# Optimization experiments

Hardware: AMD Instinct MI355X
Metric: run time of the kernel (lower is better)

The kernel has to match this reference:

```python
import jax, jax.numpy as jnp
import numpy as np

SLOPE = 25.0   # snntorch fast_sigmoid default slope
EPS = 1e-5     # BatchNorm eps
ALPHA = 1.0    # tdBN alpha
VTH_BN = 1.0   # tdBN VTH constant

@jax.custom_vjp
def spike_fn(x):
    # Heaviside forward, fast-sigmoid surrogate backward
    return (x > 0).astype(x.dtype)

def _spike_fwd(x):
    return (x > 0).astype(x.dtype), x

def _spike_bwd(x, g):
    return (g / (SLOPE * jnp.abs(x) + 1.0) ** 2,)

spike_fn.defvjp(_spike_fwd, _spike_bwd)

def setup_inputs() -> dict:
    key = jax.random.key(0)
    ks = jax.random.split(key, 4)
    B, T, F_in, F_out = 64, 64, 2048, 2048
    x = jax.random.normal(ks[0], (B, T, F_in), jnp.float32)
    mem_init = jnp.zeros((B, F_out), jnp.float32)
    # Linear params (Kaiming-uniform-ish init)
    W = jax.random.normal(ks[1], (F_out, F_in), jnp.float32) / np.sqrt(F_in)
    b = jax.random.uniform(ks[2], (F_out,), jnp.float32, -1.0, 1.0) / np.sqrt(F_in)
    # tdBN affine params
    gamma = jnp.ones((F_out,), jnp.float32)
    beta_bn = jnp.zeros((F_out,), jnp.float32)
    # LIF learnable params
    lif_beta = jnp.float32(0.9)
    thr = jnp.float32(1.0)
    return dict(x=x, mem_init=mem_init, W=W, b=b, gamma=gamma,
                beta_bn=beta_bn, lif_beta=lif_beta, thr=thr)

def reference(x, mem_init, W, b, gamma, beta_bn, lif_beta, thr):
    B, T, F_in = x.shape
    # Linear over all (batch, time) tokens at once
    h = jnp.einsum('btf,of->bto', x, W) + b  # (B, T, F_out)
    # tdBN: normalize per-feature over (batch, time), scale by alpha*VTH
    mean = h.mean(axis=(0, 1))
    var = h.var(axis=(0, 1))  # biased, matches torch BN training stats
    h = ALPHA * VTH_BN * (h - mean) / jnp.sqrt(var + EPS) * gamma + beta_bn
    # LIF (snntorch Leaky, subtract reset) scanned over time
    beta_c = jnp.clip(lif_beta, 0.0, 1.0)
    def step(mem, xt):
        # reset based on previous mem, detached (snntorch mem_reset)
        reset = jax.lax.stop_gradient((mem - thr > 0).astype(mem.dtype))
        mem_new = beta_c * mem + xt - reset * thr
        spk = spike_fn(mem_new - thr)
        return mem_new, spk
    _, spks = jax.lax.scan(step, mem_init, jnp.swapaxes(h, 0, 1))  # spks: (T, B, F)
    return jnp.swapaxes(spks, 0, 1)  # (B, T, F_out)
```

## Files before the change

kernel.cpp:

```cpp
#include <hip/hip_runtime.h>


typedef double double4v __attribute__((ext_vector_type(4)));

#define KDIM 2048
#define NDIM 2048
#define LROW 132

__global__ __launch_bounds__(256, 2) void gemm_f64_mfma2(
    const float* __restrict__ X,
    const float* __restrict__ W,
    const float* __restrict__ bias,
    double* __restrict__ H)
{
    constexpr int NT = KDIM / 16;
    __shared__ float As[2][16][LROW];
    __shared__ float Bs[2][16][LROW];

    const int tid  = threadIdx.x;
    const int lane = tid & 63;
    const int wid  = tid >> 6;
    const int lf = lane & 15, lq = lane >> 4;
    const int bm = blockIdx.x * 128, bn = blockIdx.y * 128;
    const int wr = wid >> 1, wc = wid & 1;

    double4v pd = (double4v){0.0, 0.0, 0.0, 0.0};
    pd = __builtin_amdgcn_mfma_f64_16x16x4f64(
        (double)(lane + 1), (double)((lane + 1) * (lane + 1)), pd, 0, 0, 0);
    int winner = -1;
    #pragma unroll
    for (int h = 0; h < 16; ++h) {
        const int c1 = h & 1, c2 = (h >> 1) & 1, cd = h >> 2;
        bool ok = true;
        #pragma unroll
        for (int v = 0; v < 4; ++v) {
            const int r16 = (cd == 0) ? 4 * lq + v : (cd == 1) ? lf
                          : (cd == 2) ? lq + 4 * v : lf;
            const int c16 = (cd == 0) ? lf : (cd == 1) ? 4 * lq + v
                          : (cd == 2) ? lf : lq + 4 * v;
            double s = 0.0;
            #pragma unroll
            for (int k = 0; k < 4; ++k) {
                const int i1 = c1 ? (r16 + 16 * k) : (4 * r16 + k);
                const int i2 = c2 ? (c16 + 16 * k) : (4 * c16 + k);
                s += (double)(i1 + 1) * (double)((i2 + 1) * (i2 + 1));
            }
            ok = ok && (pd[v] == s);
        }
        if (__ballot(ok) == ~0ull && winner < 0) winner = h;
    }
    if (winner < 0) winner = 0;
    const int selA = winner & 1, selB = (winner >> 1) & 1, selD = winner >> 2;

    const int rlA = selA ? lf : (lane >> 2);
    const int klA = selA ? lq : (lane & 3);
    const int rlB = selB ? lf : (lane >> 2);
    const int klB = selB ? lq : (lane & 3);
    const int baseA = klA * LROW + wr * 64 + rlA;
    const int baseB = klB * LROW + wc * 64 + rlB;

    const int arow = tid >> 1;
    const int akof = (tid & 1) * 8;
    const float* xa = X + (size_t)(bm + arow) * KDIM + akof;
    const float* wa = W + (size_t)(bn + arow) * KDIM + akof;

#define STAGE(buf, va0, va1, vb0, vb1) do { \
    As[buf][akof+0][arow]=va0.x; As[buf][akof+1][arow]=va0.y; \
    As[buf][akof+2][arow]=va0.z; As[buf][akof+3][arow]=va0.w; \
    As[buf][akof+4][arow]=va1.x; As[buf][akof+5][arow]=va1.y; \
    As[buf][akof+6][arow]=va1.z; As[buf][akof+7][arow]=va1.w; \
    Bs[buf][akof+0][arow]=vb0.x; Bs[buf][akof+1][arow]=vb0.y; \
    Bs[buf][akof+2][arow]=vb0.z; Bs[buf][akof+3][arow]=vb0.w; \
    Bs[buf][akof+4][arow]=vb1.x; Bs[buf][akof+5][arow]=vb1.y; \
    Bs[buf][akof+6][arow]=vb1.z; Bs[buf][akof+7][arow]=vb1.w; } while (0)

    double4v acc[4][4];
    #pragma unroll
    for (int t = 0; t < 4; ++t)
        #pragma unroll
        for (int u = 0; u < 4; ++u)
            acc[t][u] = (double4v){0.0, 0.0, 0.0, 0.0};

    {
        float4 a0 = *(const float4*)xa;
        float4 a1 = *(const float4*)(xa + 4);
        float4 b0 = *(const float4*)wa;
        float4 b1 = *(const float4*)(wa + 4);
        STAGE(0, a0, a1, b0, b1);
    }
    __syncthreads();

    int cur = 0;
    for (int t = 0; t < NT; ++t) {
        const bool more = (t + 1) < NT;
        float4 pa0, pa1, pb0, pb1;
        if (more) {
            const int k0 = (t + 1) * 16;
            pa0 = *(const float4*)(xa + k0);
            pa1 = *(const float4*)(xa + k0 + 4);
            pb0 = *(const float4*)(wa + k0);
            pb1 = *(const float4*)(wa + k0 + 4);
        }

        const float* Af = &As[cur][0][0];
        const float* Bf = &Bs[cur][0][0];
        #pragma unroll
        for (int ks = 0; ks < 4; ++ks) {
            const int ko = 4 * ks * LROW;
            const double fa0 = (double)Af[ko + baseA +  0];
            const double fa1 = (double)Af[ko + baseA + 16];
            const double fa2 = (double)Af[ko + baseA + 32];
            const double fa3 = (double)Af[ko + baseA + 48];
            const double fb0 = (double)Bf[ko + baseB +  0];
            const double fb1 = (double)Bf[ko + baseB + 16];
            const double fb2 = (double)Bf[ko + baseB + 32];
            const double fb3 = (double)Bf[ko + baseB + 48];
#define MM(ti, ui, av, bv) \
            acc[ti][ui] = __builtin_amdgcn_mfma_f64_16x16x4f64(av, bv, acc[ti][ui], 0, 0, 0);
            MM(0,0,fa0,fb0) MM(0,1,fa0,fb1) MM(0,2,fa0,fb2) MM(0,3,fa0,fb3)
            MM(1,0,fa1,fb0) MM(1,1,fa1,fb1) MM(1,2,fa1,fb2) MM(1,3,fa1,fb3)
            MM(2,0,fa2,fb0) MM(2,1,fa2,fb1) MM(2,2,fa2,fb2) MM(2,3,fa2,fb3)
            MM(3,0,fa3,fb0) MM(3,1,fa3,fb1) MM(3,2,fa3,fb2) MM(3,3,fa3,fb3)
#undef MM
        }

        if (more) STAGE(cur ^ 1, pa0, pa1, pb0, pb1);
        __syncthreads();
        cur ^= 1;
    }

    #pragma unroll
    for (int v = 0; v < 4; ++v) {
        const int r16 = (selD == 0) ? 4 * lq + v : (selD == 1) ? lf
                      : (selD == 2) ? lq + 4 * v : lf;
        const int c16 = (selD == 0) ? lf : (selD == 1) ? 4 * lq + v
                      : (selD == 2) ? lf : lq + 4 * v;
        #pragma unroll
        for (int t = 0; t < 4; ++t) {
            const int row = bm + wr * 64 + 16 * t + r16;
            #pragma unroll
            for (int u = 0; u < 4; ++u) {
                const int col = bn + wc * 64 + 16 * u + c16;
                H[(size_t)row * NDIM + col] = acc[t][u][v] + (double)bias[col];
            }
        }
    }
}

__global__ __launch_bounds__(256) void bn_partial(
    const double* __restrict__ H, double* __restrict__ psum, double* __restrict__ psq)
{
    constexpr int N = 2048, ROWS = 128;
    const int o  = blockIdx.x * 256 + threadIdx.x;
    const int t0 = blockIdx.y * ROWS;
    double s = 0.0, q = 0.0;
    for (int r = 0; r < ROWS; ++r) {
        double h = H[(size_t)(t0 + r) * N + o];
        s += h;
        q = fma(h, h, q);
    }
    psum[(size_t)blockIdx.y * N + o] = s;
    psq [(size_t)blockIdx.y * N + o] = q;
}

__global__ void bn_finalize(const double* __restrict__ psum, const double* __restrict__ psq,
                            double* __restrict__ meanv, double* __restrict__ varv)
{
    constexpr int N = 2048, CH = 32;
    const int o = blockIdx.x * blockDim.x + threadIdx.x;
    double s = 0.0, q = 0.0;
    for (int c = 0; c < CH; ++c) {
        s += psum[(size_t)c * N + o];
        q += psq [(size_t)c * N + o];
    }
    const double m = s / 4096.0;
    meanv[o] = m;
    varv[o]  = q / 4096.0 - m * m;
}

__global__ __launch_bounds__(256) void bn_lif(
    const double* __restrict__ H,
    const double* __restrict__ meanv, const double* __restrict__ varv,
    const float* __restrict__ gamma, const float* __restrict__ beta_bn,
    const float* __restrict__ mem_init,
    const float* __restrict__ lif_beta, const float* __restrict__ thr,
    float* __restrict__ out)
{
    constexpr int T = 64, F = 2048;
    const int gid = blockIdx.x * 256 + threadIdx.x;
    const int o = gid & (F - 1);
    const int b = gid >> 11;

    const double m      = meanv[o];
    const double invstd = 1.0 / sqrt(varv[o] + 1e-5);
    const double sc     = invstd * (double)gamma[o];
    const double sh     = (double)beta_bn[o];
    const double beta_c = fmin(fmax((double)lif_beta[0], 0.0), 1.0);
    const double th     = (double)thr[0];

    double mem = (double)mem_init[gid];
    const double* hp = H   + (size_t)b * T * F + o;
    float*        op = out + (size_t)b * T * F + o;

    for (int t = 0; t < T; ++t) {
        const double h  = hp[(size_t)t * F];
        const double xt = (h - m) * sc + sh;
        const double reset = (mem > th) ? th : 0.0;
        mem = fma(beta_c, mem, xt) - reset;
        op[(size_t)t * F] = (mem > th) ? 1.0f : 0.0f;
    }
}

extern "C" void kernel_launch(void* const* d_in, const int* in_sizes, int n_in,
                              void* d_out, int out_size, void* d_ws, size_t ws_size,
                              hipStream_t stream)
{
    const float* x        = (const float*)d_in[0];
    const float* mem_init = (const float*)d_in[1];
    const float* W        = (const float*)d_in[2];
    const float* b        = (const float*)d_in[3];
    const float* gamma    = (const float*)d_in[4];
    const float* beta_bn  = (const float*)d_in[5];
    const float* lif_beta = (const float*)d_in[6];
    const float* thr      = (const float*)d_in[7];
    float* out = (float*)d_out;

    char* ws = (char*)d_ws;
    double* H     = (double*)ws;
    double* psum  = (double*)(ws + (size_t)67108864);
    double* psq   = (double*)(ws + (size_t)67108864 + 524288);
    double* meanv = (double*)(ws + (size_t)67108864 + 2 * 524288);
    double* varv  = meanv + 2048;

    gemm_f64_mfma2<<<dim3(32, 16), 256, 0, stream>>>(x, W, b, H);
    bn_partial    <<<dim3(8, 32),  256, 0, stream>>>(H, psum, psq);
    bn_finalize   <<<8,            256, 0, stream>>>(psum, psq, meanv, varv);
    bn_lif        <<<512,          256, 0, stream>>>(H, meanv, varv, gamma, beta_bn,
                                                     mem_init, lif_beta, thr, out);
}
```

Measured before the change: 639.1 us.

## Interleave LDS tile layout for float4 fragment reads and double K-tile depth

Rearranges the shared-memory staging so the four 16-row fragments each lane needs sit next to each other. Each k-step can then fetch them with one float4 LDS read per operand instead of four scalar reads. The K tile also grows from 16 to 32, which halves the number of barriers and prefetch rounds. The trade-off is double the LDS footprint and more registers for prefetch, and removing the row padding may bring back bank conflicts on the transposed stores.

```diff
diff --git a/kernel.cpp b/kernel.cpp
--- a/kernel.cpp
+++ b/kernel.cpp
@@ -5,17 +5,18 @@
 
 #define KDIM 2048
 #define NDIM 2048
-#define LROW 132
-
-__global__ __launch_bounds__(256, 2) void gemm_f64_mfma2(
+#define BKt  32
+#define LROW 128
+
+__global__ __launch_bounds__(256, 2) void gemm_f64_mfma3(
     const float* __restrict__ X,
     const float* __restrict__ W,
     const float* __restrict__ bias,
     double* __restrict__ H)
 {
-    constexpr int NT = KDIM / 16;
-    __shared__ float As[2][16][LROW];
-    __shared__ float Bs[2][16][LROW];
+    constexpr int NT = KDIM / BKt;
+    __shared__ float As[2][BKt][LROW];
+    __shared__ float Bs[2][BKt][LROW];
 
     const int tid  = threadIdx.x;
     const int lane = tid & 63;
@@ -56,23 +57,33 @@
     const int klA = selA ? lq : (lane & 3);
     const int rlB = selB ? lf : (lane >> 2);
     const int klB = selB ? lq : (lane & 3);
-    const int baseA = klA * LROW + wr * 64 + rlA;
-    const int baseB = klB * LROW + wc * 64 + rlB;
+    const int baseA = klA * LROW + wr * 64 + rlA * 4;
+    const int baseB = klB * LROW + wc * 64 + rlB * 4;
 
     const int arow = tid >> 1;
-    const int akof = (tid & 1) * 8;
-    const float* xa = X + (size_t)(bm + arow) * KDIM + akof;
-    const float* wa = W + (size_t)(bn + arow) * KDIM + akof;
-
-#define STAGE(buf, va0, va1, vb0, vb1) do { \
-    As[buf][akof+0][arow]=va0.x; As[buf][akof+1][arow]=va0.y; \
-    As[buf][akof+2][arow]=va0.z; As[buf][akof+3][arow]=va0.w; \
-    As[buf][akof+4][arow]=va1.x; As[buf][akof+5][arow]=va1.y; \
-    As[buf][akof+6][arow]=va1.z; As[buf][akof+7][arow]=va1.w; \
-    Bs[buf][akof+0][arow]=vb0.x; Bs[buf][akof+1][arow]=vb0.y; \
-    Bs[buf][akof+2][arow]=vb0.z; Bs[buf][akof+3][arow]=vb0.w; \
-    Bs[buf][akof+4][arow]=vb1.x; Bs[buf][akof+5][arow]=vb1.y; \
-    Bs[buf][akof+6][arow]=vb1.z; Bs[buf][akof+7][arow]=vb1.w; } while (0)
+    const int kofs = (tid & 1) * 16;
+    const float* xa = X + (size_t)(bm + arow) * KDIM + kofs;
+    const float* wa = W + (size_t)(bn + arow) * KDIM + kofs;
+    const int r6  = arow & 63;
+    const int pos = (arow >> 6) * 64 + (r6 & 15) * 4 + (r6 >> 4);
+
+#define STAGE(buf, A0, A1, A2, A3, B0, B1, B2, B3) do { \
+    As[buf][kofs+ 0][pos]=A0.x; As[buf][kofs+ 1][pos]=A0.y; \
+    As[buf][kofs+ 2][pos]=A0.z; As[buf][kofs+ 3][pos]=A0.w; \
+    As[buf][kofs+ 4][pos]=A1.x; As[buf][kofs+ 5][pos]=A1.y; \
+    As[buf][kofs+ 6][pos]=A1.z; As[buf][kofs+ 7][pos]=A1.w; \
+    As[buf][kofs+ 8][pos]=A2.x; As[buf][kofs+ 9][pos]=A2.y; \
+    As[buf][kofs+10][pos]=A2.z; As[buf][kofs+11][pos]=A2.w; \
+    As[buf][kofs+12][pos]=A3.x; As[buf][kofs+13][pos]=A3.y; \
+    As[buf][kofs+14][pos]=A3.z; As[buf][kofs+15][pos]=A3.w; \
+    Bs[buf][kofs+ 0][pos]=B0.x; Bs[buf][kofs+ 1][pos]=B0.y; \
+    Bs[buf][kofs+ 2][pos]=B0.z; Bs[buf][kofs+ 3][pos]=B0.w; \
+    Bs[buf][kofs+ 4][pos]=B1.x; Bs[buf][kofs+ 5][pos]=B1.y; \
+    Bs[buf][kofs+ 6][pos]=B1.z; Bs[buf][kofs+ 7][pos]=B1.w; \
+    Bs[buf][kofs+ 8][pos]=B2.x; Bs[buf][kofs+ 9][pos]=B2.y; \
+    Bs[buf][kofs+10][pos]=B2.z; Bs[buf][kofs+11][pos]=B2.w; \
+    Bs[buf][kofs+12][pos]=B3.x; Bs[buf][kofs+13][pos]=B3.y; \
+    Bs[buf][kofs+14][pos]=B3.z; Bs[buf][kofs+15][pos]=B3.w; } while (0)
 
     double4v acc[4][4];
     #pragma unroll
@@ -82,39 +93,42 @@
             acc[t][u] = (double4v){0.0, 0.0, 0.0, 0.0};
 
     {
-        float4 a0 = *(const float4*)xa;
+        float4 a0 = *(const float4*)(xa);
         float4 a1 = *(const float4*)(xa + 4);
-        float4 b0 = *(const float4*)wa;
+        float4 a2 = *(const float4*)(xa + 8);
+        float4 a3 = *(const float4*)(xa + 12);
+        float4 b0 = *(const float4*)(wa);
         float4 b1 = *(const float4*)(wa + 4);
-        STAGE(0, a0, a1, b0, b1);
+        float4 b2 = *(const float4*)(wa + 8);
+        float4 b3 = *(const float4*)(wa + 12);
+        STAGE(0, a0, a1, a2, a3, b0, b1, b2, b3);
     }
     __syncthreads();
 
     int cur = 0;
     for (int t = 0; t < NT; ++t) {
         const bool more = (t + 1) < NT;
-        float4 pa0, pa1, pb0, pb1;
+        float4 pa0, pa1, pa2, pa3, pb0, pb1, pb2, pb3;
         if (more) {
-            const int k0 = (t + 1) * 16;
+            const int k0 = (t + 1) * BKt;
             pa0 = *(const float4*)(xa + k0);
             pa1 = *(const float4*)(xa + k0 + 4);
+            pa2 = *(const float4*)(xa + k0 + 8);
+            pa3 = *(const float4*)(xa + k0 + 12);
             pb0 = *(const float4*)(wa + k0);
             pb1 = *(const float4*)(wa + k0 + 4);
+            pb2 = *(const float4*)(wa + k0 + 8);
+            pb3 = *(const float4*)(wa + k0 + 12);
         }
 
         const float* Af = &As[cur][0][0];
         const float* Bf = &Bs[cur][0][0];
         #pragma unroll
-        for (int ks = 0; ks < 4; ++ks) {
-            const int ko = 4 * ks * LROW;
-            const double fa0 = (double)Af[ko + baseA +  0];
-            const double fa1 = (double)Af[ko + baseA + 16];
-            const double fa2 = (double)Af[ko + baseA + 32];
-            const double fa3 = (double)Af[ko + baseA + 48];
-            const double fb0 = (double)Bf[ko + baseB +  0];
-            const double fb1 = (double)Bf[ko + baseB + 16];
-            const double fb2 = (double)Bf[ko + baseB + 32];
-            const double fb3 = (double)Bf[ko + baseB + 48];
+        for (int ks = 0; ks < 8; ++ks) {
+            const float4 fa = *(const float4*)&Af[4 * ks * LROW + baseA];
+            const float4 fb = *(const float4*)&Bf[4 * ks * LROW + baseB];
+            const double fa0 = fa.x, fa1 = fa.y, fa2 = fa.z, fa3 = fa.w;
+            const double fb0 = fb.x, fb1 = fb.y, fb2 = fb.z, fb3 = fb.w;
 #define MM(ti, ui, av, bv) \
             acc[ti][ui] = __builtin_amdgcn_mfma_f64_16x16x4f64(av, bv, acc[ti][ui], 0, 0, 0);
             MM(0,0,fa0,fb0) MM(0,1,fa0,fb1) MM(0,2,fa0,fb2) MM(0,3,fa0,fb3)
@@ -124,7 +138,7 @@
 #undef MM
         }
 
-        if (more) STAGE(cur ^ 1, pa0, pa1, pb0, pb1);
+        if (more) STAGE(cur ^ 1, pa0, pa1, pa2, pa3, pb0, pb1, pb2, pb3);
         __syncthreads();
         cur ^= 1;
     }
@@ -232,7 +246,7 @@
     double* meanv = (double*)(ws + (size_t)67108864 + 2 * 524288);
     double* varv  = meanv + 2048;
 
-    gemm_f64_mfma2<<<dim3(32, 16), 256, 0, stream>>>(x, W, b, H);
+    gemm_f64_mfma3<<<dim3(32, 16), 256, 0, stream>>>(x, W, b, H);
     bn_partial    <<<dim3(8, 32),  256, 0, stream>>>(H, psum, psq);
     bn_finalize   <<<8,            256, 0, stream>>>(psum, psq, meanv, varv);
     bn_lif        <<<512,          256, 0, stream>>>(H, meanv, varv, gamma, beta_bn,
```

Result: no change. 637.2 us (-0.3%).

## Shrink GEMM tile to 64x128 with vectorized interleaved LDS fragment loads

Applied to the files above, without the earlier changes.

Halves the M tile of the FP64 MFMA GEMM from 128 to 64 rows, doubling the grid to 64x16 blocks and raising launch bounds to 4 blocks per SM. The shared-memory layout is permuted so each lane's per-k-step A and B fragments are contiguous, allowing float2/float4 LDS reads instead of scalar loads. This aims to raise occupancy and cut LDS instruction count, at the cost of lower arithmetic intensity per block (fewer MFMAs per loaded element) and more global traffic for W.

```diff
diff --git a/kernel.cpp b/kernel.cpp
--- a/kernel.cpp
+++ b/kernel.cpp
@@ -5,24 +5,26 @@
 
 #define KDIM 2048
 #define NDIM 2048
-#define LROW 132
-
-__global__ __launch_bounds__(256, 2) void gemm_f64_mfma2(
+#define BKt  16
+#define LRA  68
+#define LRB  136
+
+__global__ __launch_bounds__(256, 4) void gemm_f64_mfma4(
     const float* __restrict__ X,
     const float* __restrict__ W,
     const float* __restrict__ bias,
     double* __restrict__ H)
 {
-    constexpr int NT = KDIM / 16;
-    __shared__ float As[2][16][LROW];
-    __shared__ float Bs[2][16][LROW];
+    constexpr int NT = KDIM / BKt;
+    __shared__ float As[2][BKt][LRA];
+    __shared__ float Bs[2][BKt][LRB];
 
     const int tid  = threadIdx.x;
     const int lane = tid & 63;
     const int wid  = tid >> 6;
     const int lf = lane & 15, lq = lane >> 4;
-    const int bm = blockIdx.x * 128, bn = blockIdx.y * 128;
-    const int wr = wid >> 1, wc = wid & 1;
+    const int bm = blockIdx.x * 64, bn = blockIdx.y * 128;
+    const int wrow = wid >> 1, wcol = wid & 1;
 
     double4v pd = (double4v){0.0, 0.0, 0.0, 0.0};
     pd = __builtin_amdgcn_mfma_f64_16x16x4f64(
@@ -56,48 +58,48 @@
     const int klA = selA ? lq : (lane & 3);
     const int rlB = selB ? lf : (lane >> 2);
     const int klB = selB ? lq : (lane & 3);
-    const int baseA = klA * LROW + wr * 64 + rlA;
-    const int baseB = klB * LROW + wc * 64 + rlB;
-
-    const int arow = tid >> 1;
-    const int akof = (tid & 1) * 8;
-    const float* xa = X + (size_t)(bm + arow) * KDIM + akof;
-    const float* wa = W + (size_t)(bn + arow) * KDIM + akof;
-
-#define STAGE(buf, va0, va1, vb0, vb1) do { \
-    As[buf][akof+0][arow]=va0.x; As[buf][akof+1][arow]=va0.y; \
-    As[buf][akof+2][arow]=va0.z; As[buf][akof+3][arow]=va0.w; \
-    As[buf][akof+4][arow]=va1.x; As[buf][akof+5][arow]=va1.y; \
-    As[buf][akof+6][arow]=va1.z; As[buf][akof+7][arow]=va1.w; \
-    Bs[buf][akof+0][arow]=vb0.x; Bs[buf][akof+1][arow]=vb0.y; \
-    Bs[buf][akof+2][arow]=vb0.z; Bs[buf][akof+3][arow]=vb0.w; \
-    Bs[buf][akof+4][arow]=vb1.x; Bs[buf][akof+5][arow]=vb1.y; \
-    Bs[buf][akof+6][arow]=vb1.z; Bs[buf][akof+7][arow]=vb1.w; } while (0)
-
-    double4v acc[4][4];
+    const int baseA = klA * LRA + rlA * 4 + wrow * 2;
+    const int baseB = klB * LRB + wcol * 64 + rlB * 4;
+
+    const int aRow = tid >> 2;
+    const int aKof = (tid & 3) << 2;
+    const int bRow = tid >> 1;
+    const int bKof = (tid & 1) << 3;
+    const float* xa = X + (size_t)(bm + aRow) * KDIM + aKof;
+    const float* wa = W + (size_t)(bn + bRow) * KDIM + bKof;
+    const int posA = (aRow & 15) * 4 + (aRow >> 4);
+    const int posB = (bRow >> 6) * 64 + (bRow & 15) * 4 + ((bRow >> 4) & 3);
+
+#define STAGE(buf, A0, B0, B1) do { \
+    As[buf][aKof + 0][posA] = A0.x; As[buf][aKof + 1][posA] = A0.y; \
+    As[buf][aKof + 2][posA] = A0.z; As[buf][aKof + 3][posA] = A0.w; \
+    Bs[buf][bKof + 0][posB] = B0.x; Bs[buf][bKof + 1][posB] = B0.y; \
+    Bs[buf][bKof + 2][posB] = B0.z; Bs[buf][bKof + 3][posB] = B0.w; \
+    Bs[buf][bKof + 4][posB] = B1.x; Bs[buf][bKof + 5][posB] = B1.y; \
+    Bs[buf][bKof + 6][posB] = B1.z; Bs[buf][bKof + 7][posB] = B1.w; } while (0)
+
+    double4v acc[2][4];
     #pragma unroll
-    for (int t = 0; t < 4; ++t)
+    for (int t = 0; t < 2; ++t)
         #pragma unroll
         for (int u = 0; u < 4; ++u)
             acc[t][u] = (double4v){0.0, 0.0, 0.0, 0.0};
 
     {
-        float4 a0 = *(const float4*)xa;
-        float4 a1 = *(const float4*)(xa + 4);
-        float4 b0 = *(const float4*)wa;
+        float4 a0 = *(const float4*)(xa);
+        float4 b0 = *(const float4*)(wa);
         float4 b1 = *(const float4*)(wa + 4);
-        STAGE(0, a0, a1, b0, b1);
+        STAGE(0, a0, b0, b1);
     }
     __syncthreads();
 
     int cur = 0;
     for (int t = 0; t < NT; ++t) {
         const bool more = (t + 1) < NT;
-        float4 pa0, pa1, pb0, pb1;
+        float4 pa0, pb0, pb1;
         if (more) {
-            const int k0 = (t + 1) * 16;
+            const int k0 = (t + 1) * BKt;
             pa0 = *(const float4*)(xa + k0);
-            pa1 = *(const float4*)(xa + k0 + 4);
             pb0 = *(const float4*)(wa + k0);
             pb1 = *(const float4*)(wa + k0 + 4);
         }
@@ -106,25 +108,18 @@
         const float* Bf = &Bs[cur][0][0];
         #pragma unroll
         for (int ks = 0; ks < 4; ++ks) {
-            const int ko = 4 * ks * LROW;
-            const double fa0 = (double)Af[ko + baseA +  0];
-            const double fa1 = (double)Af[ko + baseA + 16];
-            const double fa2 = (double)Af[ko + baseA + 32];
-            const double fa3 = (double)Af[ko + baseA + 48];
-            const double fb0 = (double)Bf[ko + baseB +  0];
-            const double fb1 = (double)Bf[ko + baseB + 16];
-            const double fb2 = (double)Bf[ko + baseB + 32];
-            const double fb3 = (double)Bf[ko + baseB + 48];
+            const float2 fa = *(const float2*)&Af[4 * ks * LRA + baseA];
+            const float4 fb = *(const float4*)&Bf[4 * ks * LRB + baseB];
+            const double fa0 = fa.x, fa1 = fa.y;
+            const double fb0 = fb.x, fb1 = fb.y, fb2 = fb.z, fb3 = fb.w;
 #define MM(ti, ui, av, bv) \
             acc[ti][ui] = __builtin_amdgcn_mfma_f64_16x16x4f64(av, bv, acc[ti][ui], 0, 0, 0);
             MM(0,0,fa0,fb0) MM(0,1,fa0,fb1) MM(0,2,fa0,fb2) MM(0,3,fa0,fb3)
             MM(1,0,fa1,fb0) MM(1,1,fa1,fb1) MM(1,2,fa1,fb2) MM(1,3,fa1,fb3)
-            MM(2,0,fa2,fb0) MM(2,1,fa2,fb1) MM(2,2,fa2,fb2) MM(2,3,fa2,fb3)
-            MM(3,0,fa3,fb0) MM(3,1,fa3,fb1) MM(3,2,fa3,fb2) MM(3,3,fa3,fb3)
 #undef MM
         }
 
-        if (more) STAGE(cur ^ 1, pa0, pa1, pb0, pb1);
+        if (more) STAGE(cur ^ 1, pa0, pb0, pb1);
         __syncthreads();
         cur ^= 1;
     }
@@ -136,11 +131,11 @@
         const int c16 = (selD == 0) ? lf : (selD == 1) ? 4 * lq + v
                       : (selD == 2) ? lf : lq + 4 * v;
         #pragma unroll
-        for (int t = 0; t < 4; ++t) {
-            const int row = bm + wr * 64 + 16 * t + r16;
+        for (int t = 0; t < 2; ++t) {
+            const int row = bm + wrow * 32 + 16 * t + r16;
             #pragma unroll
             for (int u = 0; u < 4; ++u) {
-                const int col = bn + wc * 64 + 16 * u + c16;
+                const int col = bn + wcol * 64 + 16 * u + c16;
                 H[(size_t)row * NDIM + col] = acc[t][u][v] + (double)bias[col];
             }
         }
@@ -232,7 +227,7 @@
     double* meanv = (double*)(ws + (size_t)67108864 + 2 * 524288);
     double* varv  = meanv + 2048;
 
-    gemm_f64_mfma2<<<dim3(32, 16), 256, 0, stream>>>(x, W, b, H);
+    gemm_f64_mfma4<<<dim3(64, 16), 256, 0, stream>>>(x, W, b, H);
     bn_partial    <<<dim3(8, 32),  256, 0, stream>>>(H, psum, psq);
     bn_finalize   <<<8,            256, 0, stream>>>(psum, psq, meanv, varv);
     bn_lif        <<<512,          256, 0, stream>>>(H, meanv, varv, gamma, beta_bn,
```

After: 665.3 us. 4.1% more time.
